# Optimization experiments

Hardware: AMD Instinct MI355X
Metric: run time of the kernel (lower is better)

Reference implementation:

```python
import jax, jax.numpy as jnp
import numpy as np

VOCAB, DIM, LAYERS, HEADS, FF, SEQ, BATCH = 32000, 1024, 4, 16, 4096, 2048, 2
HD = DIM // HEADS
EPS = 1e-6
ROPE_BASE = 10000.0


def setup_inputs() -> dict:
    key = jax.random.key(0)
    ks = jax.random.split(key, 10)
    std = 0.02
    return {
        "input_ids": jax.random.randint(ks[0], (BATCH, SEQ), 0, VOCAB, dtype=jnp.int32),
        "emb": jax.random.normal(ks[1], (VOCAB, DIM), jnp.float32) * std,
        "qkv_w": jax.random.normal(ks[2], (LAYERS, 3 * DIM, DIM), jnp.float32) * std,
        "out_w": jax.random.normal(ks[3], (LAYERS, DIM, DIM), jnp.float32) * std,
        "fc1_w": jax.random.normal(ks[4], (LAYERS, FF, DIM), jnp.float32) * std,
        "fc2_w": jax.random.normal(ks[5], (LAYERS, DIM, FF), jnp.float32) * std,
        "norm1_s": jnp.ones((LAYERS, DIM), jnp.float32),
        "norm2_s": jnp.ones((LAYERS, DIM), jnp.float32),
        "normf_s": jnp.ones((DIM,), jnp.float32),
        "lm_w": jax.random.normal(ks[6], (VOCAB, DIM), jnp.float32) * std,
    }


def _rms(x, scale):
    return x * jax.lax.rsqrt(jnp.mean(x * x, axis=-1, keepdims=True) + EPS) * scale


def _rope_tables(seq_len):
    inv_freq = 1.0 / (ROPE_BASE ** (jnp.arange(0, HD, 2, dtype=jnp.float32) / HD))
    freqs = jnp.arange(seq_len, dtype=jnp.float32)[:, None] * inv_freq[None, :]  # [S, HD/2]
    emb = jnp.concatenate([freqs, freqs], axis=-1)  # [S, HD]
    return jnp.cos(emb), jnp.sin(emb)


def _rotate_half(x):
    x1, x2 = jnp.split(x, 2, axis=-1)
    return jnp.concatenate([-x2, x1], axis=-1)


def _attention(h, qkv_w, out_w, cos, sin, mask):
    B, S, _ = h.shape
    qkv = jnp.einsum('bsd,ed->bse', h, qkv_w)  # [B, S, 3*DIM]
    qkv = qkv.reshape(B, S, 3, HEADS, HD).transpose(2, 0, 3, 1, 4)  # [3, B, H, S, hd]
    q, k, v = qkv[0], qkv[1], qkv[2]
    q = q * cos + _rotate_half(q) * sin
    k = k * cos + _rotate_half(k) * sin
    scores = jnp.einsum('bhqd,bhkd->bhqk', q, k) * (HD ** -0.5)
    scores = jnp.where(mask, scores, -jnp.inf)
    attn = jax.nn.softmax(scores, axis=-1)
    out = jnp.einsum('bhqk,bhkd->bhqd', attn, v)
    out = out.transpose(0, 2, 1, 3).reshape(B, S, DIM)
    return jnp.einsum('bsd,ed->bse', out, out_w)


def reference(input_ids, emb, qkv_w, out_w, fc1_w, fc2_w, norm1_s, norm2_s, normf_s, lm_w):
    B, S = input_ids.shape
    x = emb[input_ids]  # [B, S, DIM]
    cos, sin = _rope_tables(S)
    mask = jnp.tril(jnp.ones((S, S), dtype=bool))  # causal
    for l in range(LAYERS):
        x = x + _attention(_rms(x, norm1_s[l]), qkv_w[l], out_w[l], cos, sin, mask)
        h = _rms(x, norm2_s[l])
        ff = jnp.einsum('bsf,df->bsd', jax.nn.silu(jnp.einsum('bsd,fd->bsf', h, fc1_w[l])), fc2_w[l])
        x = x + ff
    logits = jnp.einsum('bsd,vd->bsv', _rms(x, normf_s), lm_w)
    return logits
```

## Files before the change

### kernel.cpp

```cpp
#include <hip/hip_runtime.h>

using u16 = unsigned short;
using u32 = unsigned int;
using bf16x8 = __attribute__((ext_vector_type(8))) __bf16;
using u16x8  = __attribute__((ext_vector_type(8))) u16;
using f32x4  = __attribute__((ext_vector_type(4))) float;
using u32x4  = __attribute__((ext_vector_type(4))) u32;

#define SEQ    2048
#define BATCH  2
#define DIM    1024
#define HEADS  16
#define HD     64
#define FF     4096
#define LAYERS 4
#define VOCAB  32000
#define ROWS   (BATCH*SEQ)

__device__ __forceinline__ u16 f2bf(float f) {
  u32 u = __float_as_uint(f);
  u += 0x7fffu + ((u >> 16) & 1u);
  return (u16)(u >> 16);
}
__device__ __forceinline__ float bf2f(u16 h) { return __uint_as_float(((u32)h) << 16); }

__device__ __forceinline__ void gload_lds16(const u16* g, u16* l) {
  __builtin_amdgcn_global_load_lds(
      (__attribute__((address_space(1))) void*)(u16*)g,
      (__attribute__((address_space(3))) void*)l, 16, 0, 0);
}

constexpr int BM = 128, BN = 128, BK = 32;

template<int EPI>
__global__ __launch_bounds__(256)
void gemm_nt(const u16* __restrict__ A, const u16* __restrict__ Bw,
             float* __restrict__ Cf, u16* __restrict__ Cb,
             int M, int N, int K, int KH)
{
  __shared__ __align__(16) u16 As[2][BM*BK];
  __shared__ __align__(16) u16 Bs[2][BN*BK];
  const int tid  = threadIdx.x;
  const int wid  = tid >> 6;
  const int lane = tid & 63;
  const int bn = blockIdx.x, bm = blockIdx.y;
  const int wm = wid >> 1, wn = wid & 1;

  if constexpr (EPI == 5) {
    const int z = blockIdx.z;
    A  += (size_t)z * KH;
    Bw += (size_t)z * KH;
    Cf += (size_t)z * M * N;
  }

  f32x4 acc[4][4] = {};

  const int lr = lane >> 2;
  const int lk = (lane & 3) * 8;
  const u16* Ag0 = A  + (size_t)(bm*BM + wid*16     + lr)*K + lk;
  const u16* Ag1 = A  + (size_t)(bm*BM + (wid+4)*16 + lr)*K + lk;
  const u16* Bg0 = Bw + (size_t)(bn*BN + wid*16     + lr)*K + lk;
  const u16* Bg1 = Bw + (size_t)(bn*BN + (wid+4)*16 + lr)*K + lk;

  auto STG = [&](int buf, int k0) {
    gload_lds16(Ag0 + k0, &As[buf][ wid   *512]);
    gload_lds16(Ag1 + k0, &As[buf][(wid+4)*512]);
    gload_lds16(Bg0 + k0, &Bs[buf][ wid   *512]);
    gload_lds16(Bg1 + k0, &Bs[buf][(wid+4)*512]);
  };

  const int aoff = (wm*64 + (lane & 15))*BK + (lane >> 4)*8;
  const int boff = (wn*64 + (lane & 15))*BK + (lane >> 4)*8;

  STG(0, 0);
  const int nt = KH / BK;
  for (int t = 0; t < nt; ++t) {
    __syncthreads();
    if (t + 1 < nt) STG((t+1) & 1, (t+1)*BK);
    const u16* Asf = &As[t & 1][aoff];
    const u16* Bsf = &Bs[t & 1][boff];
    bf16x8 af[4], bfr[4];
    #pragma unroll
    for (int m = 0; m < 4; ++m) af[m] = *(const bf16x8*)(Asf + m*16*BK);
    #pragma unroll
    for (int n = 0; n < 4; ++n) bfr[n] = *(const bf16x8*)(Bsf + n*16*BK);
    #pragma unroll
    for (int m = 0; m < 4; ++m)
      #pragma unroll
      for (int n = 0; n < 4; ++n)
        acc[m][n] = __builtin_amdgcn_mfma_f32_16x16x32_bf16(af[m], bfr[n], acc[m][n], 0, 0, 0);
  }

  const int row0 = bm*BM + wm*64 + (lane >> 4)*4;
  const int col0 = bn*BN + wn*64 + (lane & 15);
  #pragma unroll
  for (int m = 0; m < 4; ++m) {
    #pragma unroll
    for (int n = 0; n < 4; ++n) {
      #pragma unroll
      for (int r = 0; r < 4; ++r) {
        const size_t idx = (size_t)(row0 + m*16 + r)*N + (col0 + n*16);
        const float v = acc[m][n][r];
        if constexpr (EPI == 0)      Cf[idx] = v;
        else if constexpr (EPI == 1) Cf[idx] += v;
        else if constexpr (EPI == 2) Cb[idx] = f2bf(v / (1.f + __expf(-v)));
        else if constexpr (EPI == 5) Cf[idx] = v;
        else                         Cb[idx] = f2bf(v);
      }
    }
  }
}

__global__ __launch_bounds__(256)
void residual_add2(float* __restrict__ x, const float* __restrict__ p0,
                   const float* __restrict__ p1)
{
  const int i = blockIdx.x*256 + threadIdx.x;
  const float4 a = ((const float4*)x)[i];
  const float4 b = ((const float4*)p0)[i];
  const float4 c = ((const float4*)p1)[i];
  float4 o;
  o.x = a.x + b.x + c.x;
  o.y = a.y + b.y + c.y;
  o.z = a.z + b.z + c.z;
  o.w = a.w + b.w + c.w;
  ((float4*)x)[i] = o;
}

#define GPHASE(buf, q, STAGE_STMT, WAITV)                                     \
  {                                                                           \
    if ((q) == 0) {                                                           \
      _Pragma("unroll") for (int n = 0; n < 4; ++n)                           \
        _Pragma("unroll") for (int ks = 0; ks < 2; ++ks)                      \
          bfrag[n][ks] = ldsB((buf), wn*64 + n*16, ks);                       \
    }                                                                         \
    bf16x8 afrag[2][2];                                                       \
    _Pragma("unroll") for (int mi = 0; mi < 2; ++mi)                          \
      _Pragma("unroll") for (int ks = 0; ks < 2; ++ks)                        \
        afrag[mi][ks] = ldsA((buf), wm*128 + (q)*32 + mi*16, ks);             \
    STAGE_STMT;                                                               \
    __builtin_amdgcn_s_barrier();                                             \
    asm volatile("" ::: "memory");                                            \
    __builtin_amdgcn_s_setprio(1);                                            \
    _Pragma("unroll") for (int mi = 0; mi < 2; ++mi)                          \
      _Pragma("unroll") for (int n = 0; n < 4; ++n)                           \
        _Pragma("unroll") for (int ks = 0; ks < 2; ++ks)                      \
          acc[(q)*2+mi][n] = __builtin_amdgcn_mfma_f32_16x16x32_bf16(         \
              afrag[mi][ks], bfrag[n][ks], acc[(q)*2+mi][n], 0, 0, 0);        \
    __builtin_amdgcn_s_setprio(0);                                            \
    if ((WAITV) == 1) asm volatile("s_waitcnt vmcnt(6)" ::: "memory");        \
    if ((WAITV) == 2) asm volatile("s_waitcnt vmcnt(0)" ::: "memory");        \
    __builtin_amdgcn_s_barrier();                                             \
    asm volatile("" ::: "memory");                                            \
  }

template<int EPI>
__global__ __launch_bounds__(512, 2)
void gemm_nt_256(const u16* __restrict__ A, const u16* __restrict__ Bw,
                 float* __restrict__ Cf, u16* __restrict__ Cb,
                 u16* __restrict__ qbo, u16* __restrict__ kbo,
                 u16* __restrict__ vto, const float* __restrict__ tab,
                 int M, int N, int K, int nbm)
{
  __shared__ __align__(16) u16 lds[2][2][256*64];
  const int tid = threadIdx.x, wid = tid >> 6, lane = tid & 63;
  const int nwg = gridDim.x;
  const int swz = (blockIdx.x & 7)*(nwg >> 3) + (blockIdx.x >> 3);
  const int bm = swz % nbm, bn = swz / nbm;
  const int wm = wid >> 2, wn = wid & 3;

  f32x4 acc[8][4] = {};

  const int lrow = lane >> 3;
  const int lkel = ((lane & 7) ^ lrow) * 8;
  const u16* Abase = A  + (size_t)(bm*256)*K + lkel;
  const u16* Bbase = Bw + (size_t)(bn*256)*K + lkel;
  auto stageA = [&](int buf, int ha, int t) {
    const int r0 = ha*64 + 8*wid, r1 = 128 + ha*64 + 8*wid;
    const size_t ko = (size_t)t*64;
    gload_lds16(Abase + (size_t)(r0 + lrow)*K + ko, &lds[buf][0][r0*64]);
    gload_lds16(Abase + (size_t)(r1 + lrow)*K + ko, &lds[buf][0][r1*64]);
  };
  auto stageB = [&](int buf, int hb, int t) {
    const int r0 = hb*128 + 8*wid, r1 = hb*128 + 64 + 8*wid;
    const size_t ko = (size_t)t*64;
    gload_lds16(Bbase + (size_t)(r0 + lrow)*K + ko, &lds[buf][1][r0*64]);
    gload_lds16(Bbase + (size_t)(r1 + lrow)*K + ko, &lds[buf][1][r1*64]);
  };

  const int frow = lane & 15, g = lane >> 4;
  auto ldsA = [&](int buf, int rowbase, int ks) -> bf16x8 {
    return *(const bf16x8*)&lds[buf][0][(rowbase + frow)*64 + ((ks*4 + g) ^ (lane & 7))*8];
  };
  auto ldsB = [&](int buf, int rowbase, int ks) -> bf16x8 {
    return *(const bf16x8*)&lds[buf][1][(rowbase + frow)*64 + ((ks*4 + g) ^ (lane & 7))*8];
  };

  bf16x8 bfrag[4][2];
  const int NT = K / 64;

  stageB(0,0,0); stageB(0,1,0); stageA(0,0,0); stageA(0,1,0);
  stageB(1,0,1); stageB(1,1,1); stageA(1,0,1);
  asm volatile("s_waitcnt vmcnt(6)" ::: "memory");
  __builtin_amdgcn_s_barrier();
  asm volatile("" ::: "memory");

  for (int i = 0; i < NT/2 - 1; ++i) {
    const int t0 = 2*i;
    GPHASE(0, 0, stageA(1,1,t0+1), 0)
    GPHASE(0, 1, stageB(0,0,t0+2), 0)
    GPHASE(0, 2, stageB(0,1,t0+2), 0)
    GPHASE(0, 3, stageA(0,0,t0+2), 1)
    GPHASE(1, 0, stageA(0,1,t0+2), 0)
    GPHASE(1, 1, stageB(1,0,t0+3), 0)
    GPHASE(1, 2, stageB(1,1,t0+3), 0)
    GPHASE(1, 3, stageA(1,0,t0+3), 1)
  }
  GPHASE(0, 0, stageA(1,1,NT-1), 0)
  GPHASE(0, 1, ((void)0), 0)
  GPHASE(0, 2, ((void)0), 0)
  GPHASE(0, 3, ((void)0), 2)
  GPHASE(1, 0, ((void)0), 0)
  GPHASE(1, 1, ((void)0), 0)
  GPHASE(1, 2, ((void)0), 0)
  GPHASE(1, 3, ((void)0), 0)

  if constexpr (EPI == 4) {
    const int hc = bn*4 + wn;
    const int which = hc >> 4, h = hc & 15;
    const int brow0 = bm*256 + wm*128 + g*4;
    const int b = brow0 >> 11;
    const int bh = b*HEADS + h;
    if (which == 2) {
      #pragma unroll
      for (int mrep = 0; mrep < 8; ++mrep) {
        const int s = (brow0 + mrep*16) & (SEQ-1);
        #pragma unroll
        for (int n = 0; n < 4; ++n) {
          const int d = frow + n*16;
          ushort4 pk;
          pk.x = f2bf(acc[mrep][n][0]); pk.y = f2bf(acc[mrep][n][1]);
          pk.z = f2bf(acc[mrep][n][2]); pk.w = f2bf(acc[mrep][n][3]);
          *(ushort4*)&vto[((size_t)bh*64 + d)*SEQ + s] = pk;
        }
      }
    } else {
      u16* outb = (which == 0) ? qbo : kbo;
      const float qs = (which == 0) ? 0.125f : 1.f;
      #pragma unroll
      for (int mrep = 0; mrep < 8; ++mrep) {
        #pragma unroll
        for (int rr = 0; rr < 4; ++rr) {
          const int s = (brow0 + mrep*16 + rr) & (SEQ-1);
          const float c0 = tab[s*64 + frow],      s0v = tab[s*64 + 32 + frow];
          const float c1 = tab[s*64 + 16 + frow], s1v = tab[s*64 + 48 + frow];
          const float x0 = acc[mrep][0][rr], x1 = acc[mrep][1][rr];
          const float x2 = acc[mrep][2][rr], x3 = acc[mrep][3][rr];
          u16* orow = outb + ((size_t)bh*SEQ + s)*64;
          orow[frow]      = f2bf((x0*c0 - x2*s0v)*qs);
          orow[frow + 32] = f2bf((x2*c0 + x0*s0v)*qs);
          orow[frow + 16] = f2bf((x1*c1 - x3*s1v)*qs);
          orow[frow + 48] = f2bf((x3*c1 + x1*s1v)*qs);
        }
      }
    }
  } else {
    const int row0 = bm*256 + wm*128 + g*4;
    const int col0 = bn*256 + wn*64 + frow;
    #pragma unroll
    for (int mrep = 0; mrep < 8; ++mrep) {
      #pragma unroll
      for (int n = 0; n < 4; ++n) {
        #pragma unroll
        for (int r = 0; r < 4; ++r) {
          const size_t idx = (size_t)(row0 + mrep*16 + r)*N + (col0 + n*16);
          const float v = acc[mrep][n][r];
          if constexpr (EPI == 0)      Cf[idx] = v;
          else if constexpr (EPI == 2) Cb[idx] = f2bf(v / (1.f + __expf(-v)));
        }
      }
    }
  }
}

__global__ void cvt_f32_bf16(const float* __restrict__ in, u16* __restrict__ out, int n4)
{
  const int i = blockIdx.x*256 + threadIdx.x;
  if (i >= n4) return;
  const float4 v = ((const float4*)in)[i];
  ushort4 o;
  o.x = f2bf(v.x); o.y = f2bf(v.y); o.z = f2bf(v.z); o.w = f2bf(v.w);
  ((ushort4*)out)[i] = o;
}

__global__ void embed_gather(const int* __restrict__ ids, const float* __restrict__ emb,
                             float* __restrict__ x)
{
  const int row = blockIdx.x, t = threadIdx.x;
  const int id = ids[row];
  ((float4*)(x + (size_t)row*DIM))[t] = ((const float4*)(emb + (size_t)id*DIM))[t];
}

__global__ __launch_bounds__(256)
void rmsnorm_bf16(const float* __restrict__ x, const float* __restrict__ scale,
                  u16* __restrict__ out)
{
  const int row = blockIdx.x, t = threadIdx.x;
  const float4 v = ((const float4*)(x + (size_t)row*DIM))[t];
  float ss = v.x*v.x + v.y*v.y + v.z*v.z + v.w*v.w;
  #pragma unroll
  for (int off = 32; off; off >>= 1) ss += __shfl_xor(ss, off);
  __shared__ float red[4];
  if ((t & 63) == 0) red[t >> 6] = ss;
  __syncthreads();
  const float tot = red[0] + red[1] + red[2] + red[3];
  const float r = rsqrtf(tot * (1.f/(float)DIM) + 1e-6f);
  const float4 sc = ((const float4*)scale)[t];
  ushort4 o;
  o.x = f2bf(v.x * r * sc.x);
  o.y = f2bf(v.y * r * sc.y);
  o.z = f2bf(v.z * r * sc.z);
  o.w = f2bf(v.w * r * sc.w);
  ((ushort4*)(out + (size_t)row*DIM))[t] = o;
}

__global__ void rope_table(float* __restrict__ tab)
{
  const int idx = blockIdx.x*256 + threadIdx.x;
  const int s = idx >> 5, i = idx & 31;
  const float invf = powf(10000.f, -(float)i/32.f);
  const float f = (float)s * invf;
  tab[s*64 + i]      = cosf(f);
  tab[s*64 + 32 + i] = sinf(f);
}

__global__ __launch_bounds__(256)
void attn_fwd(const u16* __restrict__ qb, const u16* __restrict__ kb,
              const u16* __restrict__ vt, u16* __restrict__ ctx)
{
  const int wid = threadIdx.x >> 6, lane = threadIdx.x & 63;
  const int bh = blockIdx.x >> 5, j = blockIdx.x & 31;
  const int qt = (wid == 0) ? j : (wid == 1) ? 63 - j : (wid == 2) ? 64 + j : 127 - j;
  const int q0 = qt * 16;
  const int g = lane >> 4, c15 = lane & 15;

  const u16* qbase = qb + (size_t)bh*SEQ*64;
  const u16* kbase = kb + (size_t)bh*SEQ*64;
  const u16* vtb   = vt + (size_t)bh*64*SEQ;

  const bf16x8 bQ0 = *(const bf16x8*)(qbase + (size_t)(q0 + c15)*64 + g*8);
  const bf16x8 bQ1 = *(const bf16x8*)(qbase + (size_t)(q0 + c15)*64 + 32 + g*8);

  f32x4 o[4] = {};
  float m = -INFINITY, lsum = 0.f;
  const int q_abs = q0 + c15;
  const int nt = (q0 >> 5) + 1;

  for (int t = 0; t < nt; ++t) {
    const int k0 = t*32;
    const u16* kr0 = kbase + (size_t)(k0 + c15)*64 + g*8;
    const u16* kr1 = kbase + (size_t)(k0 + 16 + c15)*64 + g*8;
    const bf16x8 aK00 = *(const bf16x8*)(kr0);
    const bf16x8 aK01 = *(const bf16x8*)(kr0 + 32);
    const bf16x8 aK10 = *(const bf16x8*)(kr1);
    const bf16x8 aK11 = *(const bf16x8*)(kr1 + 32);
    const f32x4 z = {};
    f32x4 sc0 = __builtin_amdgcn_mfma_f32_16x16x32_bf16(aK00, bQ0, z, 0,0,0);
    sc0 = __builtin_amdgcn_mfma_f32_16x16x32_bf16(aK01, bQ1, sc0, 0,0,0);
    f32x4 sc1 = __builtin_amdgcn_mfma_f32_16x16x32_bf16(aK10, bQ0, z, 0,0,0);
    sc1 = __builtin_amdgcn_mfma_f32_16x16x32_bf16(aK11, bQ1, sc1, 0,0,0);

    float s0[4], s1[4];
    if (k0 + 31 > q0) {
      #pragma unroll
      for (int r = 0; r < 4; ++r) {
        s0[r] = (k0 + 4*g + r      > q_abs) ? -INFINITY : sc0[r];
        s1[r] = (k0 + 16 + 4*g + r > q_abs) ? -INFINITY : sc1[r];
      }
    } else {
      #pragma unroll
      for (int r = 0; r < 4; ++r) { s0[r] = sc0[r]; s1[r] = sc1[r]; }
    }

    float tm = fmaxf(fmaxf(fmaxf(s0[0], s0[1]), fmaxf(s0[2], s0[3])),
                     fmaxf(fmaxf(s1[0], s1[1]), fmaxf(s1[2], s1[3])));
    tm = fmaxf(tm, __shfl_xor(tm, 16));
    tm = fmaxf(tm, __shfl_xor(tm, 32));

    if (!__all(tm <= m + 8.f)) {
      const float mnew = fmaxf(m, tm);
      const float corr = __expf(m - mnew);
      lsum *= corr;
      float corrq[4];
      #pragma unroll
      for (int r = 0; r < 4; ++r) corrq[r] = __shfl(corr, 4*g + r);
      #pragma unroll
      for (int dh = 0; dh < 4; ++dh)
        #pragma unroll
        for (int r = 0; r < 4; ++r) o[dh][r] *= corrq[r];
      m = mnew;
    }

    float p0[4], p1[4];
    #pragma unroll
    for (int r = 0; r < 4; ++r) { p0[r] = __expf(s0[r] - m); p1[r] = __expf(s1[r] - m); }
    float ps = (p0[0]+p0[1]) + (p0[2]+p0[3]) + (p1[0]+p1[1]) + (p1[2]+p1[3]);
    ps += __shfl_xor(ps, 16);
    ps += __shfl_xor(ps, 32);
    lsum += ps;

    const u32 pk00 = (u32)f2bf(p0[0]) | ((u32)f2bf(p0[1]) << 16);
    const u32 pk01 = (u32)f2bf(p0[2]) | ((u32)f2bf(p0[3]) << 16);
    const u32 pk10 = (u32)f2bf(p1[0]) | ((u32)f2bf(p1[1]) << 16);
    const u32 pk11 = (u32)f2bf(p1[2]) | ((u32)f2bf(p1[3]) << 16);
    u32 w[4];
    #pragma unroll
    for (int wi = 0; wi < 4; ++wi) {
      const int src = c15 | ((((g << 1) + (wi >> 1)) & 3) << 4);
      const u32 a0 = __shfl((wi & 1) ? pk01 : pk00, src);
      const u32 a1 = __shfl((wi & 1) ? pk11 : pk10, src);
      w[wi] = (g < 2) ? a0 : a1;
    }
    const bf16x8 aP = __builtin_bit_cast(bf16x8, (u32x4){w[0], w[1], w[2], w[3]});

    #pragma unroll
    for (int dh = 0; dh < 4; ++dh) {
      const bf16x8 bV = *(const bf16x8*)(vtb + (size_t)(dh*16 + c15)*SEQ + k0 + g*8);
      o[dh] = __builtin_amdgcn_mfma_f32_16x16x32_bf16(aP, bV, o[dh], 0,0,0);
    }
  }

  float linv[4];
  #pragma unroll
  for (int r = 0; r < 4; ++r) linv[r] = 1.f / __shfl(lsum, 4*g + r);
  const int b = bh >> 4, h = bh & 15;
  #pragma unroll
  for (int r = 0; r < 4; ++r) {
    u16* crow = ctx + ((size_t)(b*SEQ + q0 + 4*g + r))*DIM + h*HD + c15;
    #pragma unroll
    for (int dh = 0; dh < 4; ++dh) crow[dh*16] = f2bf(o[dh][r] * linv[r]);
  }
}

extern "C" void kernel_launch(void* const* d_in, const int* in_sizes, int n_in,
                              void* d_out, int out_size, void* d_ws, size_t ws_size,
                              hipStream_t stream)
{
  const int*   ids   = (const int*)  d_in[0];
  const float* emb   = (const float*)d_in[1];
  const float* qkv_w = (const float*)d_in[2];
  const float* out_w = (const float*)d_in[3];
  const float* fc1_w = (const float*)d_in[4];
  const float* fc2_w = (const float*)d_in[5];
  const float* n1    = (const float*)d_in[6];
  const float* n2    = (const float*)d_in[7];
  const float* nf    = (const float*)d_in[8];
  const float* lm_w  = (const float*)d_in[9];
  float* logits = (float*)d_out;

  char* ws = (char*)d_ws;
  size_t off = 0;
  auto walloc = [&](size_t bytes) -> void* {
    void* p = ws + off;
    off += (bytes + 255) & ~(size_t)255;
    return p;
  };
  float* x     = (float*)walloc((size_t)ROWS*DIM*4);
  u16*   hbf   = (u16*)  walloc((size_t)ROWS*DIM*2);
  u16*   ctxbf = (u16*)  walloc((size_t)ROWS*DIM*2);
  u16*   gbf   = (u16*)  walloc((size_t)ROWS*FF*2);
  u16*   wq    = (u16*)  walloc((size_t)3*DIM*DIM*2);
  u16*   wo    = (u16*)  walloc((size_t)DIM*DIM*2);
  u16*   w1    = (u16*)  walloc((size_t)FF*DIM*2);
  u16*   w2    = (u16*)  walloc((size_t)DIM*FF*2);
  float* tab   = (float*)walloc((size_t)SEQ*64*4);
  float* fpart = (float*)walloc((size_t)2*ROWS*DIM*4);
  u16* qbuf = (u16*)gbf;
  u16* kbuf = qbuf + (size_t)ROWS*DIM;
  u16* vtbuf= kbuf + (size_t)ROWS*DIM;
  u16* wlm = (u16*)ctxbf;

  rope_table<<<SEQ*32/256, 256, 0, stream>>>(tab);
  embed_gather<<<ROWS, 256, 0, stream>>>(ids, emb, x);

  for (int l = 0; l < LAYERS; ++l) {
    cvt_f32_bf16<<<3*DIM*DIM/4/256, 256, 0, stream>>>(qkv_w + (size_t)l*3*DIM*DIM, wq, 3*DIM*DIM/4);
    cvt_f32_bf16<<<DIM*DIM/4/256,   256, 0, stream>>>(out_w + (size_t)l*DIM*DIM,   wo, DIM*DIM/4);
    cvt_f32_bf16<<<FF*DIM/4/256,    256, 0, stream>>>(fc1_w + (size_t)l*FF*DIM,    w1, FF*DIM/4);
    cvt_f32_bf16<<<DIM*FF/4/256,    256, 0, stream>>>(fc2_w + (size_t)l*DIM*FF,    w2, DIM*FF/4);

    rmsnorm_bf16<<<ROWS, 256, 0, stream>>>(x, n1 + l*DIM, hbf);
    gemm_nt_256<4><<<(3*DIM/256)*(ROWS/256), 512, 0, stream>>>(
        hbf, wq, nullptr, nullptr, qbuf, kbuf, vtbuf, tab, ROWS, 3*DIM, DIM, ROWS/256);
    attn_fwd<<<BATCH*HEADS*(SEQ/64), 256, 0, stream>>>(qbuf, kbuf, vtbuf, ctxbf);
    gemm_nt<1><<<dim3(DIM/BN, ROWS/BM), 256, 0, stream>>>(ctxbf, wo, x, nullptr, ROWS, DIM, DIM, DIM);

    rmsnorm_bf16<<<ROWS, 256, 0, stream>>>(x, n2 + l*DIM, hbf);
    gemm_nt_256<2><<<(FF/256)*(ROWS/256), 512, 0, stream>>>(
        hbf, w1, nullptr, gbf, nullptr, nullptr, nullptr, nullptr, ROWS, FF, DIM, ROWS/256);
    gemm_nt<5><<<dim3(DIM/BN, ROWS/BM, 2), 256, 0, stream>>>(gbf, w2, fpart, nullptr, ROWS, DIM, FF, FF/2);
    residual_add2<<<ROWS*DIM/4/256, 256, 0, stream>>>(x, fpart, fpart + (size_t)ROWS*DIM);
  }

  rmsnorm_bf16<<<ROWS, 256, 0, stream>>>(x, nf, hbf);
  cvt_f32_bf16<<<VOCAB*DIM/4/256, 256, 0, stream>>>(lm_w, wlm, VOCAB*DIM/4);
  gemm_nt_256<0><<<(VOCAB/256)*(ROWS/256), 512, 0, stream>>>(
      hbf, wlm, logits, nullptr, nullptr, nullptr, nullptr, nullptr, ROWS, VOCAB, DIM, ROWS/256);
}
```

Measured before the change: 1.687 ms.

## Process two key tiles per attention iteration and merge weight conversion launches

The attention loop now handles 64 keys per iteration, two 32-key tiles. K and V loads for both tiles are issued before the score MFMAs, and one online-softmax max/rescale step covers both tiles, which exposes more memory-level parallelism and halves the per-tile softmax bookkeeping. A launch bound of 4 is added to attn_fwd to steer register allocation. The four per-layer weight conversion kernels are merged into one launch to cut launch overhead. The cost is more live registers in the attention kernel, which can reduce occupancy or cause spills.

```diff
diff --git a/kernel.cpp b/kernel.cpp
--- a/kernel.cpp
+++ b/kernel.cpp
@@ -293,6 +293,23 @@
   ((ushort4*)out)[i] = o;
 }
 
+__global__ void cvt_layer(const float* __restrict__ qw, const float* __restrict__ ow,
+                          const float* __restrict__ f1, const float* __restrict__ f2,
+                          u16* __restrict__ wq, u16* __restrict__ wo,
+                          u16* __restrict__ w1, u16* __restrict__ w2)
+{
+  int i = blockIdx.x*256 + threadIdx.x;
+  const float* src; u16* dst;
+  if (i < 786432)       { src = qw; dst = wq; }
+  else if (i < 1048576) { src = ow; dst = wo; i -= 786432; }
+  else if (i < 2097152) { src = f1; dst = w1; i -= 1048576; }
+  else                  { src = f2; dst = w2; i -= 2097152; }
+  const float4 v = ((const float4*)src)[i];
+  ushort4 o;
+  o.x = f2bf(v.x); o.y = f2bf(v.y); o.z = f2bf(v.z); o.w = f2bf(v.w);
+  ((ushort4*)dst)[i] = o;
+}
+
 __global__ void embed_gather(const int* __restrict__ ids, const float* __restrict__ emb,
                              float* __restrict__ x)
 {
@@ -334,7 +351,7 @@
   tab[s*64 + 32 + i] = sinf(f);
 }
 
-__global__ __launch_bounds__(256)
+__global__ __launch_bounds__(256, 4)
 void attn_fwd(const u16* __restrict__ qb, const u16* __restrict__ kb,
               const u16* __restrict__ vt, u16* __restrict__ ctx)
 {
@@ -354,36 +371,97 @@
   f32x4 o[4] = {};
   float m = -INFINITY, lsum = 0.f;
   const int q_abs = q0 + c15;
-  const int nt = (q0 >> 5) + 1;
-
-  for (int t = 0; t < nt; ++t) {
+  const int nt32 = (q0 >> 5) + 1;
+
+  auto mk_aP = [&](const float* p) -> bf16x8 {
+    const u32 pk00 = (u32)f2bf(p[0]) | ((u32)f2bf(p[1]) << 16);
+    const u32 pk01 = (u32)f2bf(p[2]) | ((u32)f2bf(p[3]) << 16);
+    const u32 pk10 = (u32)f2bf(p[4]) | ((u32)f2bf(p[5]) << 16);
+    const u32 pk11 = (u32)f2bf(p[6]) | ((u32)f2bf(p[7]) << 16);
+    u32 w[4];
+    #pragma unroll
+    for (int wi = 0; wi < 4; ++wi) {
+      const int src = c15 | ((((g << 1) + (wi >> 1)) & 3) << 4);
+      const u32 a0 = __shfl((wi & 1) ? pk01 : pk00, src);
+      const u32 a1 = __shfl((wi & 1) ? pk11 : pk10, src);
+      w[wi] = (g < 2) ? a0 : a1;
+    }
+    return __builtin_bit_cast(bf16x8, (u32x4){w[0], w[1], w[2], w[3]});
+  };
+
+  for (int t = 0; t < nt32; t += 2) {
     const int k0 = t*32;
+    const bool haveB = (t + 1 < nt32);
+    const bool diagA = (t     == nt32 - 1);
+    const bool diagB = (t + 1 == nt32 - 1);
+
     const u16* kr0 = kbase + (size_t)(k0 + c15)*64 + g*8;
     const u16* kr1 = kbase + (size_t)(k0 + 16 + c15)*64 + g*8;
     const bf16x8 aK00 = *(const bf16x8*)(kr0);
     const bf16x8 aK01 = *(const bf16x8*)(kr0 + 32);
     const bf16x8 aK10 = *(const bf16x8*)(kr1);
     const bf16x8 aK11 = *(const bf16x8*)(kr1 + 32);
+    bf16x8 aK20{}, aK21{}, aK30{}, aK31{};
+    if (haveB) {
+      const u16* kr2 = kbase + (size_t)(k0 + 32 + c15)*64 + g*8;
+      const u16* kr3 = kbase + (size_t)(k0 + 48 + c15)*64 + g*8;
+      aK20 = *(const bf16x8*)(kr2);
+      aK21 = *(const bf16x8*)(kr2 + 32);
+      aK30 = *(const bf16x8*)(kr3);
+      aK31 = *(const bf16x8*)(kr3 + 32);
+    }
+    bf16x8 vvA[4];
+    #pragma unroll
+    for (int dh = 0; dh < 4; ++dh)
+      vvA[dh] = *(const bf16x8*)(vtb + (size_t)(dh*16 + c15)*SEQ + k0 + g*8);
+
     const f32x4 z = {};
     f32x4 sc0 = __builtin_amdgcn_mfma_f32_16x16x32_bf16(aK00, bQ0, z, 0,0,0);
     sc0 = __builtin_amdgcn_mfma_f32_16x16x32_bf16(aK01, bQ1, sc0, 0,0,0);
     f32x4 sc1 = __builtin_amdgcn_mfma_f32_16x16x32_bf16(aK10, bQ0, z, 0,0,0);
     sc1 = __builtin_amdgcn_mfma_f32_16x16x32_bf16(aK11, bQ1, sc1, 0,0,0);
-
-    float s0[4], s1[4];
-    if (k0 + 31 > q0) {
+    f32x4 sc2 = z, sc3 = z;
+    if (haveB) {
+      sc2 = __builtin_amdgcn_mfma_f32_16x16x32_bf16(aK20, bQ0, z, 0,0,0);
+      sc2 = __builtin_amdgcn_mfma_f32_16x16x32_bf16(aK21, bQ1, sc2, 0,0,0);
+      sc3 = __builtin_amdgcn_mfma_f32_16x16x32_bf16(aK30, bQ0, z, 0,0,0);
+      sc3 = __builtin_amdgcn_mfma_f32_16x16x32_bf16(aK31, bQ1, sc3, 0,0,0);
+    }
+    bf16x8 vvB[4] = {};
+    if (haveB) {
+      #pragma unroll
+      for (int dh = 0; dh < 4; ++dh)
+        vvB[dh] = *(const bf16x8*)(vtb + (size_t)(dh*16 + c15)*SEQ + k0 + 32 + g*8);
+    }
+
+    float s[16];
+    if (diagA) {
       #pragma unroll
       for (int r = 0; r < 4; ++r) {
-        s0[r] = (k0 + 4*g + r      > q_abs) ? -INFINITY : sc0[r];
-        s1[r] = (k0 + 16 + 4*g + r > q_abs) ? -INFINITY : sc1[r];
+        s[r]   = (k0 + 4*g + r      > q_abs) ? -INFINITY : sc0[r];
+        s[4+r] = (k0 + 16 + 4*g + r > q_abs) ? -INFINITY : sc1[r];
       }
     } else {
       #pragma unroll
-      for (int r = 0; r < 4; ++r) { s0[r] = sc0[r]; s1[r] = sc1[r]; }
-    }
-
-    float tm = fmaxf(fmaxf(fmaxf(s0[0], s0[1]), fmaxf(s0[2], s0[3])),
-                     fmaxf(fmaxf(s1[0], s1[1]), fmaxf(s1[2], s1[3])));
+      for (int r = 0; r < 4; ++r) { s[r] = sc0[r]; s[4+r] = sc1[r]; }
+    }
+    if (!haveB) {
+      #pragma unroll
+      for (int r = 0; r < 8; ++r) s[8+r] = -INFINITY;
+    } else if (diagB) {
+      #pragma unroll
+      for (int r = 0; r < 4; ++r) {
+        s[8+r]  = (k0 + 32 + 4*g + r > q_abs) ? -INFINITY : sc2[r];
+        s[12+r] = (k0 + 48 + 4*g + r > q_abs) ? -INFINITY : sc3[r];
+      }
+    } else {
+      #pragma unroll
+      for (int r = 0; r < 4; ++r) { s[8+r] = sc2[r]; s[12+r] = sc3[r]; }
+    }
+
+    float tm = s[0];
+    #pragma unroll
+    for (int r = 1; r < 16; ++r) tm = fmaxf(tm, s[r]);
     tm = fmaxf(tm, __shfl_xor(tm, 16));
     tm = fmaxf(tm, __shfl_xor(tm, 32));
 
@@ -401,32 +479,25 @@
       m = mnew;
     }
 
-    float p0[4], p1[4];
-    #pragma unroll
-    for (int r = 0; r < 4; ++r) { p0[r] = __expf(s0[r] - m); p1[r] = __expf(s1[r] - m); }
-    float ps = (p0[0]+p0[1]) + (p0[2]+p0[3]) + (p1[0]+p1[1]) + (p1[2]+p1[3]);
+    float p[16];
+    #pragma unroll
+    for (int r = 0; r < 16; ++r) p[r] = __expf(s[r] - m);
+    float ps = 0.f;
+    #pragma unroll
+    for (int r = 0; r < 16; ++r) ps += p[r];
     ps += __shfl_xor(ps, 16);
     ps += __shfl_xor(ps, 32);
     lsum += ps;
 
-    const u32 pk00 = (u32)f2bf(p0[0]) | ((u32)f2bf(p0[1]) << 16);
-    const u32 pk01 = (u32)f2bf(p0[2]) | ((u32)f2bf(p0[3]) << 16);
-    const u32 pk10 = (u32)f2bf(p1[0]) | ((u32)f2bf(p1[1]) << 16);
-    const u32 pk11 = (u32)f2bf(p1[2]) | ((u32)f2bf(p1[3]) << 16);
-    u32 w[4];
-    #pragma unroll
-    for (int wi = 0; wi < 4; ++wi) {
-      const int src = c15 | ((((g << 1) + (wi >> 1)) & 3) << 4);
-      const u32 a0 = __shfl((wi & 1) ? pk01 : pk00, src);
-      const u32 a1 = __shfl((wi & 1) ? pk11 : pk10, src);
-      w[wi] = (g < 2) ? a0 : a1;
-    }
-    const bf16x8 aP = __builtin_bit_cast(bf16x8, (u32x4){w[0], w[1], w[2], w[3]});
-
-    #pragma unroll
-    for (int dh = 0; dh < 4; ++dh) {
-      const bf16x8 bV = *(const bf16x8*)(vtb + (size_t)(dh*16 + c15)*SEQ + k0 + g*8);
-      o[dh] = __builtin_amdgcn_mfma_f32_16x16x32_bf16(aP, bV, o[dh], 0,0,0);
+    const bf16x8 aPA = mk_aP(&p[0]);
+    #pragma unroll
+    for (int dh = 0; dh < 4; ++dh)
+      o[dh] = __builtin_amdgcn_mfma_f32_16x16x32_bf16(aPA, vvA[dh], o[dh], 0,0,0);
+    if (haveB) {
+      const bf16x8 aPB = mk_aP(&p[8]);
+      #pragma unroll
+      for (int dh = 0; dh < 4; ++dh)
+        o[dh] = __builtin_amdgcn_mfma_f32_16x16x32_bf16(aPB, vvB[dh], o[dh], 0,0,0);
     }
   }
 
@@ -484,10 +555,10 @@
   embed_gather<<<ROWS, 256, 0, stream>>>(ids, emb, x);
 
   for (int l = 0; l < LAYERS; ++l) {
-    cvt_f32_bf16<<<3*DIM*DIM/4/256, 256, 0, stream>>>(qkv_w + (size_t)l*3*DIM*DIM, wq, 3*DIM*DIM/4);
-    cvt_f32_bf16<<<DIM*DIM/4/256,   256, 0, stream>>>(out_w + (size_t)l*DIM*DIM,   wo, DIM*DIM/4);
-    cvt_f32_bf16<<<FF*DIM/4/256,    256, 0, stream>>>(fc1_w + (size_t)l*FF*DIM,    w1, FF*DIM/4);
-    cvt_f32_bf16<<<DIM*FF/4/256,    256, 0, stream>>>(fc2_w + (size_t)l*DIM*FF,    w2, DIM*FF/4);
+    cvt_layer<<<3145728/256, 256, 0, stream>>>(
+        qkv_w + (size_t)l*3*DIM*DIM, out_w + (size_t)l*DIM*DIM,
+        fc1_w + (size_t)l*FF*DIM,    fc2_w + (size_t)l*DIM*FF,
+        wq, wo, w1, w2);
 
     rmsnorm_bf16<<<ROWS, 256, 0, stream>>>(x, n1 + l*DIM, hbf);
     gemm_nt_256<4><<<(3*DIM/256)*(ROWS/256), 512, 0, stream>>>(
```

Result: no change. 1.656 ms (-1.8%).
